# Kernel tuning notes

Measured on AMD Instinct MI355X. Metric: run time of the kernel, lower is better.

The kernel has to match this reference:

```python
import jax, jax.numpy as jnp
import numpy as np

B, S, D, H = 8, 1024, 512, 8
DH = D // H
LN_EPS = 1e-3  # keras LayerNormalization default epsilon


def positional_embeddings(s, d):
    # Faithful to the (non-standard) source formula:
    # even index k: sin(pos / 10000**(2k/d)); odd index k: cos(pos / 10000**(2k/d))
    k = jnp.arange(d, dtype=jnp.float32)
    pos = jnp.arange(s, dtype=jnp.float32)[:, None]
    angle = pos / jnp.power(10000.0, 2.0 * k / d)  # [s, d]
    return jnp.where((jnp.arange(d) % 2) == 0, jnp.sin(angle), jnp.cos(angle))


def layer_norm(x, gamma, beta):
    mu = jnp.mean(x, axis=-1, keepdims=True)
    var = jnp.mean(jnp.square(x - mu), axis=-1, keepdims=True)
    return (x - mu) * jax.lax.rsqrt(var + LN_EPS) * gamma + beta


def split_heads(x):
    # np.split(x, H, axis=-1) == contiguous last-dim chunks == this reshape
    b, s, d = x.shape
    return x.reshape(b, s, H, DH).transpose(0, 2, 1, 3)  # [B,H,S,DH]


def merge_heads(x):
    b, h, s, dh = x.shape
    return x.transpose(0, 2, 1, 3).reshape(b, s, h * dh)


def sdp_attention(q, k, v):
    # NOTE: source scales by N_HEADS (=8), not sqrt(d_head) -- kept faithful.
    scores = jnp.einsum('bhqd,bhkd->bhqk', q, k) / float(H)
    attn = jax.nn.softmax(scores, axis=-1)
    return jnp.einsum('bhqk,bhkd->bhqd', attn, v)


def mhsa(x, Wq, Wk, Wv):
    q = split_heads(x @ Wq)
    k = split_heads(x @ Wk)
    v = split_heads(x @ Wv)
    return merge_heads(sdp_attention(q, k, v))


def enc_dec_attention(enc_out):
    # Source sets queries = keys = encoder_output with NO linear projections;
    # values is unbound in the source (bug) -- we take V = encoder_output too.
    q = split_heads(enc_out)
    return merge_heads(sdp_attention(q, q, q))


def setup_inputs() -> dict:
    key = jax.random.key(0)
    ks = jax.random.split(key, 12)
    p = lambda i: jax.random.normal(ks[i], (D, D), dtype=jnp.float32) * 0.05
    return {
        'padded_encoded_input_docs': jax.random.normal(ks[0], (B, S, D), dtype=jnp.float32),
        'padded_encoded_output_docs': jax.random.normal(ks[1], (B, S, D), dtype=jnp.float32),
        'Wq_e': p(2), 'Wk_e': p(3), 'Wv_e': p(4), 'Wff_e': p(5),
        'g_e': jnp.ones((D,), jnp.float32), 'b_e': jnp.zeros((D,), jnp.float32),
        'Wq_d': p(6), 'Wk_d': p(7), 'Wv_d': p(8), 'Wff_d': p(9),
        'g_d': jnp.ones((D,), jnp.float32), 'b_d': jnp.zeros((D,), jnp.float32),
    }


def reference(padded_encoded_input_docs, padded_encoded_output_docs,
              Wq_e, Wk_e, Wv_e, Wff_e, g_e, b_e,
              Wq_d, Wk_d, Wv_d, Wff_d, g_d, b_d):
    pos = positional_embeddings(S, D).astype(padded_encoded_input_docs.dtype)

    # Encoder
    enc_in = padded_encoded_input_docs + pos
    sa_e = mhsa(enc_in, Wq_e, Wk_e, Wv_e)
    inter_e = enc_in + layer_norm(sa_e, g_e, b_e)
    enc_out = enc_in + inter_e @ Wff_e  # residual from encoder_input (as in source)

    # Decoder (single shared LN layer, reused twice, as in source)
    dec_in = padded_encoded_output_docs + pos
    sa_d = mhsa(dec_in, Wq_d, Wk_d, Wv_d)
    i1 = dec_in + layer_norm(sa_d, g_d, b_d)
    eda = enc_dec_attention(enc_out)
    # source bug kept: second LN is applied to self_attention_output again
    i2 = i1 + layer_norm(sa_d, g_d, b_d)
    dec_out = eda @ Wff_d + i2
    return dec_out
```

## Files before the change

kernel.cpp:

```cpp
#include <hip/hip_runtime.h>
#include <hip/hip_bf16.h>
#include <cstdint>

#define B_  8
#define S_  1024
#define D_  512
#define H_  8
#define DH_ 64
#define M_  (B_*S_)

typedef __attribute__((ext_vector_type(8))) short bf16x8;
typedef __attribute__((ext_vector_type(4))) float f32x4;

__device__ __forceinline__ ushort f2b(float x) {
    union { float f; uint32_t u; } c; c.f = x;
    uint32_t r = (c.u + 0x7FFFu + ((c.u >> 16) & 1u)) >> 16;
    return (ushort)r;
}

__global__ __launch_bounds__(256) void wconv_kernel(
    const float* __restrict__ w0, const float* __restrict__ w1,
    const float* __restrict__ w2, const float* __restrict__ w3,
    const float* __restrict__ w4, const float* __restrict__ w5,
    const float* __restrict__ w6, const float* __restrict__ w7,
    ushort* __restrict__ out)
{
    const float* srcs[8] = {w0,w1,w2,w3,w4,w5,w6,w7};
    int w = blockIdx.y;
    const float* src = srcs[w];
    int idx = blockIdx.x * 256 + threadIdx.x;
    int n = idx >> 9, k = idx & 511;
    out[(size_t)w * (512*512) + idx] = f2b(src[k * 512 + n]);
}

__global__ __launch_bounds__(256) void addpos_kernel(
    const float* __restrict__ x, float* __restrict__ of, ushort* __restrict__ ob)
{
    int idx = (blockIdx.x * 256 + threadIdx.x) * 4;
    int col = idx & 511;
    int s   = (idx >> 9) & 1023;
    float4 xv = *(const float4*)(x + idx);
    const float* xs = (const float*)&xv;
    float o[4];
#pragma unroll
    for (int j = 0; j < 4; ++j) {
        int k = col + j;
        float e = __expf(-(float)k * (2.0f * 9.210340371976184f / 512.0f));
        float ang = (float)s * e;
        float pv = (k & 1) ? cosf(ang) : sinf(ang);
        o[j] = xs[j] + pv;
    }
    *(float4*)(of + idx) = make_float4(o[0], o[1], o[2], o[3]);
    ushort4 ub; ub.x = f2b(o[0]); ub.y = f2b(o[1]); ub.z = f2b(o[2]); ub.w = f2b(o[3]);
    *(ushort4*)(ob + idx) = ub;
}

template<int ADD_RESID, int OUT_F32, int OUT_B16, int OUT_T>
__global__ __launch_bounds__(256) void gemm_kernel(
    const ushort* __restrict__ A, const ushort* __restrict__ Wt,
    const float* __restrict__ resid,
    float* __restrict__ outf, ushort* __restrict__ outb, ushort* __restrict__ outt)
{
    __shared__ ushort As[128][72];
    __shared__ ushort Bs[64][72];
    const int t    = threadIdx.x;
    const int m0   = blockIdx.x * 128;
    const int n0   = blockIdx.y * 64;
    const int wid  = t >> 6;
    const int lane = t & 63;
    const int lr   = lane & 15;
    const int lg   = lane >> 4;

    f32x4 acc[2][4];
#pragma unroll
    for (int mf = 0; mf < 2; ++mf)
#pragma unroll
        for (int nf = 0; nf < 4; ++nf) acc[mf][nf] = (f32x4){0.f,0.f,0.f,0.f};

    for (int k0 = 0; k0 < 512; k0 += 64) {
        __syncthreads();
#pragma unroll
        for (int i = 0; i < 4; ++i) {
            int c = t + 256 * i;
            int row = c >> 3, seg = c & 7;
            *(uint4*)&As[row][seg*8] =
                *(const uint4*)&A[(size_t)(m0+row)*512 + k0 + seg*8];
        }
#pragma unroll
        for (int i = 0; i < 2; ++i) {
            int c = t + 256 * i;
            int row = c >> 3, seg = c & 7;
            *(uint4*)&Bs[row][seg*8] =
                *(const uint4*)&Wt[(size_t)(n0+row)*512 + k0 + seg*8];
        }
        __syncthreads();
#pragma unroll
        for (int ks = 0; ks < 2; ++ks) {
            bf16x8 a[2], b[4];
            a[0] = *(const bf16x8*)&As[wid*32 +      lr][ks*32 + lg*8];
            a[1] = *(const bf16x8*)&As[wid*32 + 16 + lr][ks*32 + lg*8];
#pragma unroll
            for (int nf = 0; nf < 4; ++nf)
                b[nf] = *(const bf16x8*)&Bs[nf*16 + lr][ks*32 + lg*8];
#pragma unroll
            for (int mf = 0; mf < 2; ++mf)
#pragma unroll
                for (int nf = 0; nf < 4; ++nf)
                    acc[mf][nf] = __builtin_amdgcn_mfma_f32_16x16x32_bf16(
                        a[mf], b[nf], acc[mf][nf], 0, 0, 0);
        }
    }

#pragma unroll
    for (int mf = 0; mf < 2; ++mf)
#pragma unroll
        for (int nf = 0; nf < 4; ++nf) {
            float vv[4];
#pragma unroll
            for (int r = 0; r < 4; ++r) {
                int m = m0 + wid*32 + mf*16 + lg*4 + r;
                int n = n0 + nf*16 + lr;
                float v = acc[mf][nf][r];
                if (ADD_RESID) v += resid[(size_t)m*512 + n];
                vv[r] = v;
                if (OUT_F32) outf[(size_t)m*512 + n] = v;
                if (OUT_B16) outb[(size_t)m*512 + n] = f2b(v);
            }
            if (OUT_T) {
                int m = m0 + wid*32 + mf*16 + lg*4;
                int bb = m >> 10, sl = m & 1023;
                int h  = n0 >> 6;
                int dl = nf*16 + lr;
                ushort4 u;
                u.x = f2b(vv[0]); u.y = f2b(vv[1]); u.z = f2b(vv[2]); u.w = f2b(vv[3]);
                *(ushort4*)&outt[(((size_t)bb*8 + h)*64 + dl)*1024 + sl] = u;
            }
        }
}

template<int OUT_B16, int CSHIFT>
__global__ __launch_bounds__(256) void attn_kernel(
    const ushort* __restrict__ Qb, const ushort* __restrict__ Kb,
    const ushort* __restrict__ Vt,
    float* __restrict__ outf, ushort* __restrict__ outb)
{
    __shared__ ushort Ps[4][32][72];

    const int t    = threadIdx.x;
    const int bh   = blockIdx.x;
    const int b    = bh >> 3, h = bh & 7;
    const int q0   = blockIdx.y * 128;
    const int wid  = t >> 6;
    const int lane = t & 63;
    const int lr   = lane & 15;
    const int lg   = lane >> 4;

    const ushort* Q  = Qb + (size_t)b * S_ * D_ + h * DH_;
    const ushort* K  = Kb + (size_t)b * S_ * D_ + h * DH_;
    const ushort* Vh = Vt + (size_t)bh * DH_ * S_;

    bf16x8 qf[2][2];
#pragma unroll
    for (int mf = 0; mf < 2; ++mf)
#pragma unroll
        for (int ks = 0; ks < 2; ++ks)
            qf[mf][ks] = *(const bf16x8*)&Q[(size_t)(q0 + wid*32 + mf*16 + lr)*D_ + ks*32 + lg*8];

    f32x4 o[2][4];
#pragma unroll
    for (int mf = 0; mf < 2; ++mf)
#pragma unroll
        for (int df = 0; df < 4; ++df) o[mf][df] = (f32x4){0.f,0.f,0.f,0.f};
    float psum[2][4] = {{0.f,0.f,0.f,0.f},{0.f,0.f,0.f,0.f}};

#pragma unroll 2
    for (int kt = 0; kt < 16; ++kt) {
        const int kk0 = kt * 64;

        f32x4 s[2][4];
#pragma unroll
        for (int mf = 0; mf < 2; ++mf)
#pragma unroll
            for (int nf = 0; nf < 4; ++nf) s[mf][nf] = (f32x4){0.f,0.f,0.f,0.f};
#pragma unroll
        for (int ks = 0; ks < 2; ++ks)
#pragma unroll
            for (int nf = 0; nf < 4; ++nf) {
                bf16x8 kf = *(const bf16x8*)&K[(size_t)(kk0 + nf*16 + lr)*D_ + ks*32 + lg*8];
                s[0][nf] = __builtin_amdgcn_mfma_f32_16x16x32_bf16(qf[0][ks], kf, s[0][nf], 0,0,0);
                s[1][nf] = __builtin_amdgcn_mfma_f32_16x16x32_bf16(qf[1][ks], kf, s[1][nf], 0,0,0);
            }

        asm volatile("s_waitcnt lgkmcnt(0)" ::: "memory");

#pragma unroll
        for (int mf = 0; mf < 2; ++mf)
#pragma unroll
            for (int nf = 0; nf < 4; ++nf)
#pragma unroll
                for (int r = 0; r < 4; ++r) {
                    float pv = __expf(s[mf][nf][r] * 0.125f - (float)CSHIFT);
                    psum[mf][r] += pv;
                    Ps[wid][mf*16 + lg*4 + r][nf*16 + lr] = f2b(pv);
                }
        asm volatile("s_waitcnt lgkmcnt(0)" ::: "memory");

#pragma unroll
        for (int ks2 = 0; ks2 < 2; ++ks2) {
            bf16x8 pa0 = *(const bf16x8*)&Ps[wid][     lr][ks2*32 + lg*8];
            bf16x8 pa1 = *(const bf16x8*)&Ps[wid][16 + lr][ks2*32 + lg*8];
#pragma unroll
            for (int df = 0; df < 4; ++df) {
                bf16x8 vf = *(const bf16x8*)&Vh[(size_t)(df*16 + lr)*S_ + kk0 + ks2*32 + lg*8];
                o[0][df] = __builtin_amdgcn_mfma_f32_16x16x32_bf16(pa0, vf, o[0][df], 0,0,0);
                o[1][df] = __builtin_amdgcn_mfma_f32_16x16x32_bf16(pa1, vf, o[1][df], 0,0,0);
            }
        }
    }

#pragma unroll
    for (int mf = 0; mf < 2; ++mf)
#pragma unroll
        for (int r = 0; r < 4; ++r) {
#pragma unroll
            for (int xm = 1; xm <= 8; xm <<= 1)
                psum[mf][r] += __shfl_xor(psum[mf][r], xm);
        }

#pragma unroll
    for (int mf = 0; mf < 2; ++mf)
#pragma unroll
        for (int r = 0; r < 4; ++r) {
            float inv = 1.0f / psum[mf][r];
            int q = q0 + wid*32 + mf*16 + lg*4 + r;
#pragma unroll
            for (int df = 0; df < 4; ++df) {
                int d = df*16 + lr;
                float v = o[mf][df][r] * inv;
                size_t off = ((size_t)b * S_ + q) * D_ + h * DH_ + d;
                if (OUT_B16) outb[off] = f2b(v);
                else         outf[off] = v;
            }
        }
}

template<int MODE>
__global__ __launch_bounds__(256) void ln_kernel(
    const float* __restrict__ x, const float* __restrict__ res,
    const float* __restrict__ g, const float* __restrict__ bta,
    float* __restrict__ outf, ushort* __restrict__ outb)
{
    const int row = blockIdx.x;
    const int t = threadIdx.x;
    const size_t rb = (size_t)row * 512;
    float v0 = x[rb + t], v1 = x[rb + t + 256];
    float s = v0 + v1, ss = v0*v0 + v1*v1;
#pragma unroll
    for (int off = 32; off; off >>= 1) {
        s  += __shfl_xor(s, off);
        ss += __shfl_xor(ss, off);
    }
    __shared__ float sh_s[4], sh_ss[4];
    if ((t & 63) == 0) { sh_s[t >> 6] = s; sh_ss[t >> 6] = ss; }
    __syncthreads();
    float tot  = sh_s[0] + sh_s[1] + sh_s[2] + sh_s[3];
    float tots = sh_ss[0] + sh_ss[1] + sh_ss[2] + sh_ss[3];
    float mu   = tot * (1.0f / 512.0f);
    float var  = tots * (1.0f / 512.0f) - mu * mu;
    float rstd = rsqrtf(var + 1e-3f);
#pragma unroll
    for (int j = 0; j < 2; ++j) {
        int c = t + j * 256;
        float v = (j == 0) ? v0 : v1;
        float y = (v - mu) * rstd * g[c] + bta[c];
        if (MODE == 0) outb[rb + c] = f2b(res[rb + c] + y);
        else           outf[rb + c] = res[rb + c] + 2.0f * y;
    }
}

extern "C" void kernel_launch(void* const* d_in, const int* in_sizes, int n_in,
                              void* d_out, int out_size, void* d_ws, size_t ws_size,
                              hipStream_t stream)
{
    const float* in_docs  = (const float*)d_in[0];
    const float* out_docs = (const float*)d_in[1];
    const float* Wq_e = (const float*)d_in[2];
    const float* Wk_e = (const float*)d_in[3];
    const float* Wv_e = (const float*)d_in[4];
    const float* Wff_e= (const float*)d_in[5];
    const float* g_e  = (const float*)d_in[6];
    const float* b_e  = (const float*)d_in[7];
    const float* Wq_d = (const float*)d_in[8];
    const float* Wk_d = (const float*)d_in[9];
    const float* Wv_d = (const float*)d_in[10];
    const float* Wff_d= (const float*)d_in[11];
    const float* g_d  = (const float*)d_in[12];
    const float* b_d  = (const float*)d_in[13];
    float* out = (float*)d_out;

    char* p = (char*)d_ws;
    auto alloc = [&](size_t bytes) { char* r = p; p += (bytes + 255) & ~255ULL; return r; };
    const size_t F = (size_t)M_ * D_ * 4;
    const size_t Bb = (size_t)M_ * D_ * 2;
    float*  enc_in_f  = (float*) alloc(F);
    float*  dec_in_f  = (float*) alloc(F);
    float*  sa_f      = (float*) alloc(F);
    float*  resid_f   = (float*) alloc(F);
    ushort* enc_in_b  = (ushort*)alloc(Bb);
    ushort* dec_in_b  = (ushort*)alloc(Bb);
    ushort* q_b       = (ushort*)alloc(Bb);
    ushort* k_b       = (ushort*)alloc(Bb);
    ushort* vt_b      = (ushort*)alloc(Bb);
    ushort* x_b       = (ushort*)alloc(Bb);
    ushort* enc_out_b = (ushort*)alloc(Bb);
    ushort* eda_b     = (ushort*)alloc(Bb);
    ushort* w_b       = (ushort*)alloc((size_t)8 * 512 * 512 * 2);
    ushort* enc_out_t = (ushort*)resid_f;

    const size_t WSZ = (size_t)512 * 512;
    dim3 blk(256);

    wconv_kernel<<<dim3(1024, 8), blk, 0, stream>>>(
        Wq_e, Wk_e, Wv_e, Wff_e, Wq_d, Wk_d, Wv_d, Wff_d, w_b);
    addpos_kernel<<<dim3(4096), blk, 0, stream>>>(in_docs, enc_in_f, enc_in_b);
    addpos_kernel<<<dim3(4096), blk, 0, stream>>>(out_docs, dec_in_f, dec_in_b);

    dim3 ggrid(M_ / 128, 512 / 64);
    dim3 agrid(64, 8);
    gemm_kernel<0,0,1,0><<<ggrid, blk, 0, stream>>>(enc_in_b, w_b + 0*WSZ, nullptr, nullptr, q_b, nullptr);
    gemm_kernel<0,0,1,0><<<ggrid, blk, 0, stream>>>(enc_in_b, w_b + 1*WSZ, nullptr, nullptr, k_b, nullptr);
    gemm_kernel<0,0,0,1><<<ggrid, blk, 0, stream>>>(enc_in_b, w_b + 2*WSZ, nullptr, nullptr, nullptr, vt_b);
    attn_kernel<0,0><<<agrid, blk, 0, stream>>>(q_b, k_b, vt_b, sa_f, nullptr);
    ln_kernel<0><<<dim3(M_), blk, 0, stream>>>(sa_f, enc_in_f, g_e, b_e, nullptr, x_b);
    gemm_kernel<1,0,1,1><<<ggrid, blk, 0, stream>>>(x_b, w_b + 3*WSZ, enc_in_f, nullptr, enc_out_b, enc_out_t);

    gemm_kernel<0,0,1,0><<<ggrid, blk, 0, stream>>>(dec_in_b, w_b + 4*WSZ, nullptr, nullptr, q_b, nullptr);
    gemm_kernel<0,0,1,0><<<ggrid, blk, 0, stream>>>(dec_in_b, w_b + 5*WSZ, nullptr, nullptr, k_b, nullptr);
    gemm_kernel<0,0,0,1><<<ggrid, blk, 0, stream>>>(dec_in_b, w_b + 6*WSZ, nullptr, nullptr, nullptr, vt_b);
    attn_kernel<0,0><<<agrid, blk, 0, stream>>>(q_b, k_b, vt_b, sa_f, nullptr);
    attn_kernel<1,40><<<agrid, blk, 0, stream>>>(enc_out_b, enc_out_b, enc_out_t, nullptr, eda_b);
    ln_kernel<1><<<dim3(M_), blk, 0, stream>>>(sa_f, dec_in_f, g_d, b_d, resid_f, nullptr);
    gemm_kernel<1,1,0,0><<<ggrid, blk, 0, stream>>>(eda_b, w_b + 7*WSZ, resid_f, out, nullptr, nullptr);
}
```

Before: 434.0 us.

## Halve attention query tile per block and double-buffer P in LDS

Each attention block now handles 64 queries with 16 rows per wave instead of 32, which doubles the grid to 1024 blocks and halves per-wave accumulator registers. V fragments are loaded before the softmax step so the global loads overlap the exp work. The P tile is double-buffered in shared memory, replacing the explicit lgkmcnt waits. In exchange, each block loads K and V twice as often relative to the queries it processes, which increases global/L2 traffic.

```diff
diff --git a/kernel.cpp b/kernel.cpp
--- a/kernel.cpp
+++ b/kernel.cpp
@@ -144,13 +144,13 @@
     const ushort* __restrict__ Vt,
     float* __restrict__ outf, ushort* __restrict__ outb)
 {
-    __shared__ ushort Ps[4][32][72];
+    __shared__ ushort Ps[4][2][16][72];
 
     const int t    = threadIdx.x;
     const int bh   = blockIdx.x;
     const int b    = bh >> 3, h = bh & 7;
-    const int q0   = blockIdx.y * 128;
-    const int wid  = t >> 6;
+    const int q0   = blockIdx.y * 64;
+    const int w    = t >> 6;
     const int lane = t & 63;
     const int lr   = lane & 15;
     const int lg   = lane >> 4;
@@ -159,89 +159,75 @@
     const ushort* K  = Kb + (size_t)b * S_ * D_ + h * DH_;
     const ushort* Vh = Vt + (size_t)bh * DH_ * S_;
 
-    bf16x8 qf[2][2];
-#pragma unroll
-    for (int mf = 0; mf < 2; ++mf)
-#pragma unroll
-        for (int ks = 0; ks < 2; ++ks)
-            qf[mf][ks] = *(const bf16x8*)&Q[(size_t)(q0 + wid*32 + mf*16 + lr)*D_ + ks*32 + lg*8];
-
-    f32x4 o[2][4];
-#pragma unroll
-    for (int mf = 0; mf < 2; ++mf)
-#pragma unroll
-        for (int df = 0; df < 4; ++df) o[mf][df] = (f32x4){0.f,0.f,0.f,0.f};
-    float psum[2][4] = {{0.f,0.f,0.f,0.f},{0.f,0.f,0.f,0.f}};
+    bf16x8 qf[2];
+#pragma unroll
+    for (int ks = 0; ks < 2; ++ks)
+        qf[ks] = *(const bf16x8*)&Q[(size_t)(q0 + w*16 + lr)*D_ + ks*32 + lg*8];
+
+    f32x4 o[4];
+#pragma unroll
+    for (int df = 0; df < 4; ++df) o[df] = (f32x4){0.f,0.f,0.f,0.f};
+    float psum[4] = {0.f, 0.f, 0.f, 0.f};
 
 #pragma unroll 2
     for (int kt = 0; kt < 16; ++kt) {
         const int kk0 = kt * 64;
-
-        f32x4 s[2][4];
-#pragma unroll
-        for (int mf = 0; mf < 2; ++mf)
-#pragma unroll
-            for (int nf = 0; nf < 4; ++nf) s[mf][nf] = (f32x4){0.f,0.f,0.f,0.f};
+        const int buf = kt & 1;
+
+        f32x4 s[4];
+#pragma unroll
+        for (int nf = 0; nf < 4; ++nf) s[nf] = (f32x4){0.f,0.f,0.f,0.f};
 #pragma unroll
         for (int ks = 0; ks < 2; ++ks)
 #pragma unroll
             for (int nf = 0; nf < 4; ++nf) {
                 bf16x8 kf = *(const bf16x8*)&K[(size_t)(kk0 + nf*16 + lr)*D_ + ks*32 + lg*8];
-                s[0][nf] = __builtin_amdgcn_mfma_f32_16x16x32_bf16(qf[0][ks], kf, s[0][nf], 0,0,0);
-                s[1][nf] = __builtin_amdgcn_mfma_f32_16x16x32_bf16(qf[1][ks], kf, s[1][nf], 0,0,0);
+                s[nf] = __builtin_amdgcn_mfma_f32_16x16x32_bf16(qf[ks], kf, s[nf], 0,0,0);
             }
 
-        asm volatile("s_waitcnt lgkmcnt(0)" ::: "memory");
-
-#pragma unroll
-        for (int mf = 0; mf < 2; ++mf)
-#pragma unroll
-            for (int nf = 0; nf < 4; ++nf)
-#pragma unroll
-                for (int r = 0; r < 4; ++r) {
-                    float pv = __expf(s[mf][nf][r] * 0.125f - (float)CSHIFT);
-                    psum[mf][r] += pv;
-                    Ps[wid][mf*16 + lg*4 + r][nf*16 + lr] = f2b(pv);
-                }
-        asm volatile("s_waitcnt lgkmcnt(0)" ::: "memory");
+        bf16x8 vf[2][4];
+#pragma unroll
+        for (int ks2 = 0; ks2 < 2; ++ks2)
+#pragma unroll
+            for (int df = 0; df < 4; ++df)
+                vf[ks2][df] = *(const bf16x8*)&Vh[(size_t)(df*16 + lr)*S_ + kk0 + ks2*32 + lg*8];
+
+#pragma unroll
+        for (int nf = 0; nf < 4; ++nf)
+#pragma unroll
+            for (int r = 0; r < 4; ++r) {
+                float pv = __expf(s[nf][r] * 0.125f - (float)CSHIFT);
+                psum[r] += pv;
+                Ps[w][buf][lg*4 + r][nf*16 + lr] = f2b(pv);
+            }
 
 #pragma unroll
         for (int ks2 = 0; ks2 < 2; ++ks2) {
-            bf16x8 pa0 = *(const bf16x8*)&Ps[wid][     lr][ks2*32 + lg*8];
-            bf16x8 pa1 = *(const bf16x8*)&Ps[wid][16 + lr][ks2*32 + lg*8];
-#pragma unroll
-            for (int df = 0; df < 4; ++df) {
-                bf16x8 vf = *(const bf16x8*)&Vh[(size_t)(df*16 + lr)*S_ + kk0 + ks2*32 + lg*8];
-                o[0][df] = __builtin_amdgcn_mfma_f32_16x16x32_bf16(pa0, vf, o[0][df], 0,0,0);
-                o[1][df] = __builtin_amdgcn_mfma_f32_16x16x32_bf16(pa1, vf, o[1][df], 0,0,0);
-            }
-        }
-    }
-
-#pragma unroll
-    for (int mf = 0; mf < 2; ++mf)
-#pragma unroll
-        for (int r = 0; r < 4; ++r) {
-#pragma unroll
-            for (int xm = 1; xm <= 8; xm <<= 1)
-                psum[mf][r] += __shfl_xor(psum[mf][r], xm);
-        }
-
-#pragma unroll
-    for (int mf = 0; mf < 2; ++mf)
-#pragma unroll
-        for (int r = 0; r < 4; ++r) {
-            float inv = 1.0f / psum[mf][r];
-            int q = q0 + wid*32 + mf*16 + lg*4 + r;
-#pragma unroll
-            for (int df = 0; df < 4; ++df) {
-                int d = df*16 + lr;
-                float v = o[mf][df][r] * inv;
-                size_t off = ((size_t)b * S_ + q) * D_ + h * DH_ + d;
-                if (OUT_B16) outb[off] = f2b(v);
-                else         outf[off] = v;
-            }
-        }
+            bf16x8 pa = *(const bf16x8*)&Ps[w][buf][lr][ks2*32 + lg*8];
+#pragma unroll
+            for (int df = 0; df < 4; ++df)
+                o[df] = __builtin_amdgcn_mfma_f32_16x16x32_bf16(pa, vf[ks2][df], o[df], 0,0,0);
+        }
+    }
+
+#pragma unroll
+    for (int r = 0; r < 4; ++r)
+#pragma unroll
+        for (int xm = 1; xm <= 8; xm <<= 1)
+            psum[r] += __shfl_xor(psum[r], xm);
+
+#pragma unroll
+    for (int r = 0; r < 4; ++r) {
+        float inv = 1.0f / psum[r];
+        int q = q0 + w*16 + lg*4 + r;
+#pragma unroll
+        for (int df = 0; df < 4; ++df) {
+            float v = o[df][r] * inv;
+            size_t off = ((size_t)b * S_ + q) * D_ + h * DH_ + df*16 + lr;
+            if (OUT_B16) outb[off] = f2b(v);
+            else         outf[off] = v;
+        }
+    }
 }
 
 template<int MODE>
@@ -326,7 +312,7 @@
     addpos_kernel<<<dim3(4096), blk, 0, stream>>>(out_docs, dec_in_f, dec_in_b);
 
     dim3 ggrid(M_ / 128, 512 / 64);
-    dim3 agrid(64, 8);
+    dim3 agrid(64, 16);
     gemm_kernel<0,0,1,0><<<ggrid, blk, 0, stream>>>(enc_in_b, w_b + 0*WSZ, nullptr, nullptr, q_b, nullptr);
     gemm_kernel<0,0,1,0><<<ggrid, blk, 0, stream>>>(enc_in_b, w_b + 1*WSZ, nullptr, nullptr, k_b, nullptr);
     gemm_kernel<0,0,0,1><<<ggrid, blk, 0, stream>>>(enc_in_b, w_b + 2*WSZ, nullptr, nullptr, nullptr, vt_b);
```

Result: slower. 600.2 us (+38.3%).
